# Kernel tuning notes

Measured on AMD Instinct MI355X. Metric: run time of the kernel, lower is better.

## Reference

```python
import jax, jax.numpy as jnp
import numpy as np

BN_EPS = 1e-5

def _square_distance(a, b):
    # a: (B,N,3), b: (B,M,3) -> (B,N,M) squared euclidean distance
    a2 = jnp.sum(a * a, axis=-1)[:, :, None]
    b2 = jnp.sum(b * b, axis=-1)[:, None, :]
    return a2 + b2 - 2.0 * jnp.einsum('bnd,bmd->bnm', a, b)

def _bn(x, gamma, beta, mean, var):
    # eval-mode batchnorm over channel (last) dim
    return (x - mean) * jax.lax.rsqrt(var + BN_EPS) * gamma + beta

def setup_inputs() -> dict:
    key = jax.random.key(0)
    ks = jax.random.split(key, 16)
    B, M, N, D, C = 4, 2048, 16384, 64, 64
    din, dout = C + D, 64
    return {
        'xyz_down': jax.random.normal(ks[0], (B, M, 3), jnp.float32),
        'xyz_up': jax.random.normal(ks[1], (B, N, 3), jnp.float32),
        'feat_down': jax.random.normal(ks[2], (B, M, D), jnp.float32),
        'feat_up': jax.random.normal(ks[3], (B, N, C), jnp.float32),
        'W1': jax.random.normal(ks[4], (din, din), jnp.float32) * 0.05,
        'b1': jax.random.normal(ks[5], (din,), jnp.float32) * 0.05,
        'bn1_gamma': jax.random.uniform(ks[6], (din,), jnp.float32, 0.5, 1.5),
        'bn1_beta': jax.random.normal(ks[7], (din,), jnp.float32) * 0.05,
        'bn1_mean': jax.random.normal(ks[8], (din,), jnp.float32) * 0.05,
        'bn1_var': jax.random.uniform(ks[9], (din,), jnp.float32, 0.5, 1.5),
        'W2': jax.random.normal(ks[10], (dout, din), jnp.float32) * 0.05,
        'b2': jax.random.normal(ks[11], (dout,), jnp.float32) * 0.05,
        'bn2_gamma': jax.random.uniform(ks[12], (dout,), jnp.float32, 0.5, 1.5),
        'bn2_beta': jax.random.normal(ks[13], (dout,), jnp.float32) * 0.05,
        'bn2_mean': jax.random.normal(ks[14], (dout,), jnp.float32) * 0.05,
        'bn2_var': jax.random.uniform(ks[15], (dout,), jnp.float32, 0.5, 1.5),
    }

def reference(xyz_down, xyz_up, feat_down, feat_up,
              W1, b1, bn1_gamma, bn1_beta, bn1_mean, bn1_var,
              W2, b2, bn2_gamma, bn2_beta, bn2_mean, bn2_var):
    dist = _square_distance(xyz_up, xyz_down)              # (B,N,M)
    dist_recip = 1.0 / (dist + 1e-8)
    weight = dist_recip / jnp.sum(dist_recip, axis=2, keepdims=True)
    # bmm-equivalent of the original broadcast-multiply-sum
    feat_interp = jnp.einsum('bnm,bmd->bnd', weight, feat_down)  # (B,N,D)
    x = jnp.concatenate([feat_up, feat_interp], axis=-1)   # (B,N,C+D)
    # Conv1d(k=1) == pointwise linear over channel dim
    x = jnp.einsum('bnc,oc->bno', x, W1) + b1
    x = jax.nn.relu(_bn(x, bn1_gamma, bn1_beta, bn1_mean, bn1_var))
    x = jnp.einsum('bnc,oc->bno', x, W2) + b2
    x = _bn(x, bn2_gamma, bn2_beta, bn2_mean, bn2_var)
    return x
```

## Files before the change

### kernel.cpp

```cpp
#include <hip/hip_runtime.h>

typedef unsigned short u16;
typedef unsigned int   u32;
typedef unsigned long long u64;

typedef __attribute__((ext_vector_type(8))) short bf16x8;
typedef __attribute__((ext_vector_type(4))) float f32x4;
typedef __attribute__((ext_vector_type(2))) float f32x2;

#define BB 4
#define MM 2048
#define NN 16384
#define DD 64

__device__ __forceinline__ u16 f2bf(float f) {
    union { float f; u32 u; } v; v.f = f;
    u32 r = v.u + 0x7fffu + ((v.u >> 16) & 1u);
    return (u16)(r >> 16);
}

__device__ __forceinline__ u32 pack_trunc(float hi, float lo) {
    union { float f; u32 u; } a, b; a.f = hi; b.f = lo;
    return __builtin_amdgcn_perm(a.u, b.u, 0x07060302);
}

__device__ __forceinline__ u32 pack_rne(float hi, float lo) {
    return (u32)f2bf(lo) | ((u32)f2bf(hi) << 16);
}

__device__ __forceinline__ bf16x8 pack8(float4 p, float4 q) {
    bf16x8 v;
    v[0] = (short)f2bf(p.x); v[1] = (short)f2bf(p.y);
    v[2] = (short)f2bf(p.z); v[3] = (short)f2bf(p.w);
    v[4] = (short)f2bf(q.x); v[5] = (short)f2bf(q.y);
    v[6] = (short)f2bf(q.z); v[7] = (short)f2bf(q.w);
    return v;
}

#define OFF_FDT   0ull
#define OFF_XYZP  1048576ull
#define OFF_W1S   1179648ull
#define OFF_W2S   1212416ull
#define OFF_BN    1228800ull
#define WS_NEED   1230336ull

__global__ __launch_bounds__(256)
void prep6_kernel(const float* __restrict__ xyz_down,
                  const float* __restrict__ feat_down,
                  const float* __restrict__ W1, const float* __restrict__ b1,
                  const float* __restrict__ g1, const float* __restrict__ be1,
                  const float* __restrict__ m1, const float* __restrict__ v1,
                  const float* __restrict__ W2, const float* __restrict__ b2,
                  const float* __restrict__ g2, const float* __restrict__ be2,
                  const float* __restrict__ m2, const float* __restrict__ v2,
                  u16* __restrict__ fdT, float4* __restrict__ xyzP,
                  u16* __restrict__ w1s, u16* __restrict__ w2s,
                  float* __restrict__ bnbuf)
{
    const int blk = blockIdx.x, t = threadIdx.x;
    if (blk < 256) {
        __shared__ u16 T[32 * 72];
        const int b = blk >> 6, m0 = (blk & 63) * 32;
        {
            const int row = t >> 3, seg = (t & 7) * 8;
            const float4* src = (const float4*)(feat_down + ((size_t)(b * MM + m0 + row)) * 64 + seg);
            float4 v0 = src[0], v1 = src[1];
            bf16x8 pk = pack8(v0, v1);
            *(bf16x8*)&T[row * 72 + seg] = pk;
        }
        __syncthreads();
        {
            const int d = t & 63, w = t >> 6;
            union { u16 h[8]; uint4 q; } o;
#pragma unroll
            for (int j = 0; j < 8; j++) o.h[j] = T[(w * 8 + j) * 72 + d];
            *(uint4*)&fdT[((size_t)(b * 64 + d)) * MM + m0 + w * 8] = o.q;
        }
    } else if (blk < 272) {
        int g = (blk - 256) * 256 + t;
        int b = g >> 10, p = g & 1023;
        const float* s = xyz_down + ((size_t)b * MM + 2 * p) * 3;
        float x0 = s[0], y0 = s[1], z0 = s[2];
        float x1 = s[3], y1 = s[4], z1 = s[5];
        float w0 = x0 * x0 + y0 * y0 + z0 * z0 + 1e-8f;
        float w1v = x1 * x1 + y1 * y1 + z1 * z1 + 1e-8f;
        xyzP[(size_t)g * 2 + 0] = make_float4(-2.f * x0, -2.f * x1, -2.f * y0, -2.f * y1);
        xyzP[(size_t)g * 2 + 1] = make_float4(-2.f * z0, -2.f * z1, w0, w1v);
    } else if (blk < 280) {
        int slot = (blk - 272) * 256 + t;
        int f = slot >> 6, l = slot & 63;
        int kg = f >> 3, ot = f & 7;
        int o = ot * 16 + (l & 15), c = kg * 32 + (l >> 4) * 8;
        const float4* src = (const float4*)(W1 + (size_t)o * 128 + c);
        bf16x8 v = pack8(src[0], src[1]);
        *(bf16x8*)&w1s[(size_t)slot * 8] = v;
    } else if (blk < 284) {
        int slot = (blk - 280) * 256 + t;
        int f = slot >> 6, l = slot & 63;
        int kg = f >> 2, ot = f & 3;
        int o = ot * 16 + (l & 15), c = kg * 32 + (l >> 4) * 8;
        const float4* src = (const float4*)(W2 + (size_t)o * 128 + c);
        bf16x8 v = pack8(src[0], src[1]);
        *(bf16x8*)&w2s[(size_t)slot * 8] = v;
    } else {
        if (t < 128) {
            float a = g1[t] * rsqrtf(v1[t] + 1e-5f);
            bnbuf[t] = a;
            bnbuf[128 + t] = (b1[t] - m1[t]) * a + be1[t];
        } else if (t < 192) {
            int o = t - 128;
            float a = g2[o] * rsqrtf(v2[o] + 1e-5f);
            bnbuf[256 + o] = a;
            bnbuf[320 + o] = (b2[o] - m2[o]) * a + be2[o];
        }
    }
}

__global__ __launch_bounds__(512, 4)
void fused8_kernel(const float* __restrict__ xyz_up,
                   const u16* __restrict__ fdT,
                   const float4* __restrict__ xyzP,
                   const float* __restrict__ feat_up,
                   const u16* __restrict__ w1s,
                   const u16* __restrict__ w2s,
                   const float* __restrict__ bnbuf,
                   float* __restrict__ out)
{
    __shared__ __align__(16) char smem[34816];
    __shared__ float bnl[384];
    u16*   const ftbuf = (u16*)smem;
    float* const xyzb  = (float*)(smem + 18432);
    u16*   const xh    = (u16*)smem;
    float* const of    = (float*)smem;

    const int tid  = threadIdx.x;
    const int b    = blockIdx.x >> 7;
    const int n0   = (blockIdx.x & 127) * 128;
    const int wave = tid >> 6;
    const int lane = tid & 63;
    const int q    = lane >> 4;
    const int nl   = lane & 15;
    const int rg   = wave & 3;
    const int h    = wave >> 2;

    if (tid < 384) bnl[tid] = bnbuf[tid];

    float ax[2], ay[2], az[2];
    f32x2 a22[2];
#pragma unroll
    for (int rt = 0; rt < 2; rt++) {
        const int row = n0 + rg * 32 + rt * 16 + nl;
        const float* xu = xyz_up + ((size_t)(b * NN + row)) * 3;
        ax[rt] = xu[0]; ay[rt] = xu[1]; az[rt] = xu[2];
        float a2 = ax[rt] * ax[rt] + ay[rt] * ay[rt] + az[rt] * az[rt];
        a22[rt] = (f32x2){a2, a2};
    }
    const f32x2 eps2 = (f32x2){1e-8f, 1e-8f};

    f32x4 acc[2][4];
#pragma unroll
    for (int rt = 0; rt < 2; rt++)
#pragma unroll
        for (int i = 0; i < 4; i++) acc[rt][i] = (f32x4){0.f, 0.f, 0.f, 0.f};
    f32x4 accd[2];
    accd[0] = (f32x4){0.f, 0.f, 0.f, 0.f};
    accd[1] = (f32x4){0.f, 0.f, 0.f, 0.f};

    bf16x8 ones;
#pragma unroll
    for (int i = 0; i < 8; i++) ones[i] = (short)0x3F80;

    const int sd = tid >> 3, sms = (tid & 7) * 8;
    const u16* fsrc = fdT + ((size_t)(b * 64 + sd)) * MM + sms;
    const float4* xsrc = xyzP + ((size_t)b * 1024 + (tid >> 1)) * 2 + (tid & 1);

    {
        *(uint4*)&ftbuf[sd * 72 + sms] = *(const uint4*)fsrc;
        if (tid < 64)
            *(float4*)&xyzb[(tid >> 1) * 12 + (tid & 1) * 4] = xsrc[0];
    }
    __syncthreads();

    for (int c = 0; c < 32; ++c) {
        const int cur = c & 1, nxt = cur ^ 1;
        const bool have_next = (c + 1) < 32;
        uint4 nf; float4 nx;
        if (have_next) {
            nf = *(const uint4*)(fsrc + (c + 1) * 64);
            if (tid < 64) nx = xsrc[(size_t)(c + 1) * 64];
        }

        u32 fr[2][4];
#pragma unroll
        for (int jp = 0; jp < 4; jp++) {
            const int pi = h * 16 + q * 4 + jp;
            const float* base = &xyzb[cur * 384 + pi * 12];
            float4 ld0 = *(const float4*)(base);
            float4 ld1 = *(const float4*)(base + 4);
            f32x2 px = (f32x2){ld0.x, ld0.y};
            f32x2 py = (f32x2){ld0.z, ld0.w};
            f32x2 pz = (f32x2){ld1.x, ld1.y};
            f32x2 pw = (f32x2){ld1.z, ld1.w};
#pragma unroll
            for (int rt = 0; rt < 2; rt++) {
                f32x2 d = __builtin_elementwise_fma(px, (f32x2){ax[rt], ax[rt]},
                          __builtin_elementwise_fma(py, (f32x2){ay[rt], ay[rt]},
                          __builtin_elementwise_fma(pz, (f32x2){az[rt], az[rt]},
                                                    pw + a22[rt])));
                d = __builtin_elementwise_max(d, eps2);
                float r0 = __builtin_amdgcn_rcpf(d.x);
                float r1 = __builtin_amdgcn_rcpf(d.y);
                fr[rt][jp] = pack_trunc(r1, r0);
            }
        }
        bf16x8 bb[4];
#pragma unroll
        for (int dt = 0; dt < 4; dt++)
            bb[dt] = *(bf16x8*)&ftbuf[cur * 4608 + (dt * 16 + nl) * 72 + h * 32 + q * 8];
#pragma unroll
        for (int rt = 0; rt < 2; rt++) {
            union { u32 u[4]; bf16x8 v; } af;
            af.u[0] = fr[rt][0]; af.u[1] = fr[rt][1];
            af.u[2] = fr[rt][2]; af.u[3] = fr[rt][3];
#pragma unroll
            for (int dt = 0; dt < 4; dt++)
                acc[rt][dt] = __builtin_amdgcn_mfma_f32_16x16x32_bf16(af.v, bb[dt], acc[rt][dt], 0, 0, 0);
            accd[rt] = __builtin_amdgcn_mfma_f32_16x16x32_bf16(af.v, ones, accd[rt], 0, 0, 0);
        }

        if (have_next) {
            *(uint4*)&ftbuf[nxt * 4608 + sd * 72 + sms] = nf;
            if (tid < 64)
                *(float4*)&xyzb[nxt * 384 + (tid >> 1) * 12 + (tid & 1) * 4] = nx;
        }
        __syncthreads();
    }

    const int fur = tid >> 2, fsg = (tid & 3) * 16;
    const float4* fup = (const float4*)(feat_up + ((size_t)(b * NN + n0 + fur)) * 64 + fsg);
    float4 f0 = fup[0], f1 = fup[1], f2 = fup[2], f3 = fup[3];

    if (h) {
#pragma unroll
        for (int rt = 0; rt < 2; rt++)
#pragma unroll
        for (int reg = 0; reg < 4; reg++) {
            int row = rg * 32 + rt * 16 + q * 4 + reg;
#pragma unroll
            for (int dt = 0; dt < 4; dt++)
                of[row * 68 + dt * 16 + nl] = acc[rt][dt][reg];
            if (nl == 0) of[row * 68 + 64] = accd[rt][reg];
        }
    }
    __syncthreads();
    if (!h) {
#pragma unroll
        for (int rt = 0; rt < 2; rt++)
#pragma unroll
        for (int reg = 0; reg < 4; reg++) {
            int row = rg * 32 + rt * 16 + q * 4 + reg;
#pragma unroll
            for (int dt = 0; dt < 4; dt++)
                acc[rt][dt][reg] += of[row * 68 + dt * 16 + nl];
            accd[rt][reg] += of[row * 68 + 64];
        }
    }
    __syncthreads();
    if (!h) {
#pragma unroll
        for (int rt = 0; rt < 2; rt++)
#pragma unroll
        for (int reg = 0; reg < 4; reg++) {
            float inv = 1.0f / accd[rt][reg];
            int row = rg * 32 + rt * 16 + q * 4 + reg;
#pragma unroll
            for (int dt = 0; dt < 4; dt++)
                xh[row * 136 + 64 + dt * 16 + nl] = f2bf(acc[rt][dt][reg] * inv);
        }
    }
    {
        uint4 o0, o1;
        o0.x = pack_rne(f0.y, f0.x); o0.y = pack_rne(f0.w, f0.z);
        o0.z = pack_rne(f1.y, f1.x); o0.w = pack_rne(f1.w, f1.z);
        o1.x = pack_rne(f2.y, f2.x); o1.y = pack_rne(f2.w, f2.z);
        o1.z = pack_rne(f3.y, f3.x); o1.w = pack_rne(f3.w, f3.z);
        uint4* xd = (uint4*)&xh[fur * 136 + fsg];
        xd[0] = o0; xd[1] = o1;
    }
    __syncthreads();

    f32x4 acc1[8];
#pragma unroll
    for (int i = 0; i < 8; i++) acc1[i] = (f32x4){0.f, 0.f, 0.f, 0.f};
#pragma unroll
    for (int kg = 0; kg < 4; kg++) {
        bf16x8 afr = *(bf16x8*)&xh[(wave * 16 + nl) * 136 + kg * 32 + q * 8];
#pragma unroll
        for (int ot = 0; ot < 8; ot++) {
            bf16x8 bf = *(const bf16x8*)(w1s + ((size_t)(kg * 8 + ot) * 64 + lane) * 8);
            acc1[ot] = __builtin_amdgcn_mfma_f32_16x16x32_bf16(afr, bf, acc1[ot], 0, 0, 0);
        }
    }
#pragma unroll
    for (int ot = 0; ot < 8; ot++) {
        int o = ot * 16 + nl;
        float aa = bnl[o], bc = bnl[128 + o];
#pragma unroll
        for (int reg = 0; reg < 4; reg++) {
            float v = fmaxf(fmaf(acc1[ot][reg], aa, bc), 0.f);
            xh[(wave * 16 + q * 4 + reg) * 136 + o] = f2bf(v);
        }
    }

    f32x4 acc2[4];
#pragma unroll
    for (int i = 0; i < 4; i++) acc2[i] = (f32x4){0.f, 0.f, 0.f, 0.f};
#pragma unroll
    for (int kg = 0; kg < 4; kg++) {
        bf16x8 afr = *(bf16x8*)&xh[(wave * 16 + nl) * 136 + kg * 32 + q * 8];
#pragma unroll
        for (int ot = 0; ot < 4; ot++) {
            bf16x8 bf = *(const bf16x8*)(w2s + ((size_t)(kg * 4 + ot) * 64 + lane) * 8);
            acc2[ot] = __builtin_amdgcn_mfma_f32_16x16x32_bf16(afr, bf, acc2[ot], 0, 0, 0);
        }
    }
#pragma unroll
    for (int ot = 0; ot < 4; ot++) {
        int o = ot * 16 + nl;
        float aa = bnl[256 + o], bc = bnl[320 + o];
#pragma unroll
        for (int reg = 0; reg < 4; reg++)
            of[(wave * 16 + q * 4 + reg) * 68 + o] = fmaf(acc2[ot][reg], aa, bc);
    }

    {
        const float4* sf = (const float4*)&of[fur * 68 + fsg];
        float4* dst = (float4*)(out + ((size_t)(b * NN + n0 + fur)) * 64 + fsg);
#pragma unroll
        for (int i = 0; i < 4; i++) dst[i] = sf[i];
    }
}

#define TN 128
#define BM 64
#define RS 72
#define FS 72

__global__ __launch_bounds__(256, 3)
void interp_kernel(const float* __restrict__ xyz_down,
                   const float* __restrict__ xyz_up,
                   const float* __restrict__ feat_down,
                   u16* __restrict__ interp_out)
{
    __shared__ u16   rbuf[TN * RS];
    __shared__ u16   ftbuf[DD * FS];
    __shared__ float xyzb[BM * 3];
    __shared__ float denp[TN * 2];
    __shared__ float invden[TN];

    const int tid = threadIdx.x;
    const int b  = blockIdx.x >> 7;
    const int n0 = (blockIdx.x & 127) * TN;

    const int nl_r = tid >> 1;
    const int half = tid & 1;
    const float* xu = xyz_up + (size_t)(b * NN + n0 + nl_r) * 3;
    const float ax = xu[0], ay = xu[1], az = xu[2];

    denp[tid] = 0.f;

    const int wave = tid >> 6;
    const int lane = tid & 63;
    const int q    = lane >> 4;
    const int nl   = lane & 15;

    f32x4 acc[2][4];
#pragma unroll
    for (int i = 0; i < 2; i++)
#pragma unroll
        for (int j = 0; j < 4; j++) acc[i][j] = (f32x4){0.f, 0.f, 0.f, 0.f};

    const int sm = (tid & 31) * 2;
    const int sd = (tid >> 5) * 8;

    for (int mc = 0; mc < MM; mc += BM) {
        __syncthreads();
        if (tid < 192) xyzb[tid] = xyz_down[(size_t)(b * MM + mc) * 3 + tid];
        {
            const float4* f0 = (const float4*)(feat_down + (size_t)(b * MM + mc + sm) * DD + sd);
            const float4* f1 = (const float4*)(feat_down + (size_t)(b * MM + mc + sm + 1) * DD + sd);
            float4 a0 = f0[0], a1 = f0[1];
            float4 b0 = f1[0], b1 = f1[1];
            float r0[8] = {a0.x, a0.y, a0.z, a0.w, a1.x, a1.y, a1.z, a1.w};
            float r1[8] = {b0.x, b0.y, b0.z, b0.w, b1.x, b1.y, b1.z, b1.w};
#pragma unroll
            for (int j = 0; j < 8; j++) {
                u32 pk = (u32)f2bf(r0[j]) | ((u32)f2bf(r1[j]) << 16);
                *(u32*)&ftbuf[(sd + j) * FS + sm] = pk;
            }
        }
        __syncthreads();
        {
            float dlc = 0.f;
#pragma unroll
            for (int s = 0; s < 4; s++) {
                bf16x8 v;
#pragma unroll
                for (int j = 0; j < 8; j++) {
                    int m = half * 32 + s * 8 + j;
                    float dx = ax - xyzb[3 * m + 0];
                    float dy = ay - xyzb[3 * m + 1];
                    float dz = az - xyzb[3 * m + 2];
                    float d = fmaf(dx, dx, fmaf(dy, dy, dz * dz)) + 1e-8f;
                    float r = __builtin_amdgcn_rcpf(d);
                    dlc += r;
                    v[j] = (short)f2bf(r);
                }
                *(bf16x8*)&rbuf[nl_r * RS + half * 32 + s * 8] = v;
            }
            denp[nl_r * 2 + half] += dlc;
        }
        __syncthreads();
        {
            const int rowbase = wave * 32;
#pragma unroll
            for (int k0 = 0; k0 < BM; k0 += 32) {
                bf16x8 a0 = *(bf16x8*)&rbuf[(rowbase + nl) * RS + k0 + q * 8];
                bf16x8 a1 = *(bf16x8*)&rbuf[(rowbase + 16 + nl) * RS + k0 + q * 8];
#pragma unroll
                for (int dt = 0; dt < 4; dt++) {
                    bf16x8 bb = *(bf16x8*)&ftbuf[(dt * 16 + nl) * FS + k0 + q * 8];
                    acc[0][dt] = __builtin_amdgcn_mfma_f32_16x16x32_bf16(a0, bb, acc[0][dt], 0, 0, 0);
                    acc[1][dt] = __builtin_amdgcn_mfma_f32_16x16x32_bf16(a1, bb, acc[1][dt], 0, 0, 0);
                }
            }
        }
    }

    __syncthreads();
    if (tid < TN) invden[tid] = 1.0f / (denp[tid * 2] + denp[tid * 2 + 1]);
    __syncthreads();
    {
        const int rowbase = wave * 32;
#pragma unroll
        for (int nt = 0; nt < 2; nt++) {
#pragma unroll
            for (int reg = 0; reg < 4; reg++) {
                int nloc = rowbase + nt * 16 + q * 4 + reg;
                float inv = invden[nloc];
                size_t gbase = (size_t)(b * NN + n0 + nloc) * DD;
#pragma unroll
                for (int dt = 0; dt < 4; dt++)
                    interp_out[gbase + dt * 16 + nl] = f2bf(acc[nt][dt][reg] * inv);
            }
        }
    }
}

#define T2 64

__global__ __launch_bounds__(256, 1)
void mlp_kernel(const float* __restrict__ feat_up,
                const u16*   __restrict__ interp,
                const float* __restrict__ W1, const float* __restrict__ b1,
                const float* __restrict__ g1, const float* __restrict__ be1,
                const float* __restrict__ m1, const float* __restrict__ v1,
                const float* __restrict__ W2, const float* __restrict__ b2,
                const float* __restrict__ g2, const float* __restrict__ be2,
                const float* __restrict__ m2, const float* __restrict__ v2,
                float* __restrict__ out)
{
    __shared__ u16 xb[T2 * 136];
    __shared__ u16 hb[T2 * 136];
    __shared__ u16 w1b[128 * 136];
    __shared__ u16 w2b[64 * 136];
    __shared__ float A1[128], Bc1[128], A2[64], Bc2[64];

    const int tid = threadIdx.x;
    const int b  = blockIdx.x >> 8;
    const int n0 = (blockIdx.x & 255) * T2;
    const int wave = tid >> 6;
    const int lane = tid & 63;
    const int q    = lane >> 4;
    const int nl   = lane & 15;

    if (tid < 128) {
        float a = g1[tid] * rsqrtf(v1[tid] + 1e-5f);
        A1[tid]  = a;
        Bc1[tid] = (b1[tid] - m1[tid]) * a + be1[tid];
    } else if (tid < 192) {
        int o = tid - 128;
        float a = g2[o] * rsqrtf(v2[o] + 1e-5f);
        A2[o]  = a;
        Bc2[o] = (b2[o] - m2[o]) * a + be2[o];
    }
    {
        const float4* src = (const float4*)(W1 + (size_t)(tid >> 1) * 128 + (tid & 1) * 64);
        u16* dst = &w1b[(tid >> 1) * 136 + (tid & 1) * 64];
#pragma unroll
        for (int i = 0; i < 8; i++)
            *(bf16x8*)(dst + 8 * i) = pack8(src[2 * i], src[2 * i + 1]);
    }
    {
        const float4* src = (const float4*)(W2 + (size_t)(tid >> 2) * 128 + (tid & 3) * 32);
        u16* dst = &w2b[(tid >> 2) * 136 + (tid & 3) * 32];
#pragma unroll
        for (int i = 0; i < 4; i++)
            *(bf16x8*)(dst + 8 * i) = pack8(src[2 * i], src[2 * i + 1]);
    }
    if (tid < 128) {
        int n = tid >> 1, hf = tid & 1;
        const float4* src = (const float4*)(feat_up + (size_t)(b * NN + n0 + n) * 64 + hf * 32);
        u16* dst = &xb[n * 136 + hf * 32];
#pragma unroll
        for (int i = 0; i < 4; i++)
            *(bf16x8*)(dst + 8 * i) = pack8(src[2 * i], src[2 * i + 1]);
    } else {
        int t2 = tid - 128;
        int n = t2 >> 1, hf = t2 & 1;
        const uint4* src = (const uint4*)(interp + (size_t)(b * NN + n0 + n) * 64 + hf * 32);
        u16* dst = &xb[n * 136 + 64 + hf * 32];
#pragma unroll
        for (int i = 0; i < 4; i++)
            *(uint4*)(dst + 8 * i) = src[i];
    }
    __syncthreads();

    f32x4 acc1[8];
#pragma unroll
    for (int i = 0; i < 8; i++) acc1[i] = (f32x4){0.f, 0.f, 0.f, 0.f};
#pragma unroll
    for (int k0 = 0; k0 < 128; k0 += 32) {
        bf16x8 a = *(bf16x8*)&xb[(wave * 16 + nl) * 136 + k0 + q * 8];
#pragma unroll
        for (int ot = 0; ot < 8; ot++) {
            bf16x8 bb = *(bf16x8*)&w1b[(ot * 16 + nl) * 136 + k0 + q * 8];
            acc1[ot] = __builtin_amdgcn_mfma_f32_16x16x32_bf16(a, bb, acc1[ot], 0, 0, 0);
        }
    }
#pragma unroll
    for (int ot = 0; ot < 8; ot++) {
        int o = ot * 16 + nl;
        float aa = A1[o], bc = Bc1[o];
#pragma unroll
        for (int reg = 0; reg < 4; reg++) {
            float v = fmaxf(fmaf(acc1[ot][reg], aa, bc), 0.f);
            hb[(wave * 16 + q * 4 + reg) * 136 + o] = f2bf(v);
        }
    }
    __syncthreads();

    f32x4 acc2[4];
#pragma unroll
    for (int i = 0; i < 4; i++) acc2[i] = (f32x4){0.f, 0.f, 0.f, 0.f};
#pragma unroll
    for (int k0 = 0; k0 < 128; k0 += 32) {
        bf16x8 a = *(bf16x8*)&hb[(wave * 16 + nl) * 136 + k0 + q * 8];
#pragma unroll
        for (int ot = 0; ot < 4; ot++) {
            bf16x8 bb = *(bf16x8*)&w2b[(ot * 16 + nl) * 136 + k0 + q * 8];
            acc2[ot] = __builtin_amdgcn_mfma_f32_16x16x32_bf16(a, bb, acc2[ot], 0, 0, 0);
        }
    }
#pragma unroll
    for (int ot = 0; ot < 4; ot++) {
        int o = ot * 16 + nl;
        float aa = A2[o], bc = Bc2[o];
#pragma unroll
        for (int reg = 0; reg < 4; reg++)
            out[(size_t)(b * NN + n0 + wave * 16 + q * 4 + reg) * 64 + o] =
                fmaf(acc2[ot][reg], aa, bc);
    }
}

extern "C" void kernel_launch(void* const* d_in, const int* in_sizes, int n_in,
                              void* d_out, int out_size, void* d_ws, size_t ws_size,
                              hipStream_t stream) {
    const float* xyz_down  = (const float*)d_in[0];
    const float* xyz_up    = (const float*)d_in[1];
    const float* feat_down = (const float*)d_in[2];
    const float* feat_up   = (const float*)d_in[3];
    const float* W1  = (const float*)d_in[4];
    const float* b1  = (const float*)d_in[5];
    const float* g1  = (const float*)d_in[6];
    const float* be1 = (const float*)d_in[7];
    const float* m1  = (const float*)d_in[8];
    const float* v1  = (const float*)d_in[9];
    const float* W2  = (const float*)d_in[10];
    const float* b2  = (const float*)d_in[11];
    const float* g2  = (const float*)d_in[12];
    const float* be2 = (const float*)d_in[13];
    const float* m2  = (const float*)d_in[14];
    const float* v2  = (const float*)d_in[15];
    float* out = (float*)d_out;
    char* ws = (char*)d_ws;

    if (ws_size >= WS_NEED) {
        u16*    fdT   = (u16*)(ws + OFF_FDT);
        float4* xyzP  = (float4*)(ws + OFF_XYZP);
        u16*    w1s   = (u16*)(ws + OFF_W1S);
        u16*    w2s   = (u16*)(ws + OFF_W2S);
        float*  bnbuf = (float*)(ws + OFF_BN);

        prep6_kernel<<<dim3(285), dim3(256), 0, stream>>>(
            xyz_down, feat_down, W1, b1, g1, be1, m1, v1,
            W2, b2, g2, be2, m2, v2, fdT, xyzP, w1s, w2s, bnbuf);
        fused8_kernel<<<dim3(BB * (NN / 128)), dim3(512), 0, stream>>>(
            xyz_up, fdT, xyzP, feat_up, w1s, w2s, bnbuf, out);
    } else {
        u16* interp = (u16*)d_ws;
        interp_kernel<<<dim3(BB * (NN / TN)), dim3(256), 0, stream>>>(
            xyz_down, xyz_up, feat_down, interp);
        mlp_kernel<<<dim3(BB * (NN / T2)), dim3(256), 0, stream>>>(
            feat_up, interp, W1, b1, g1, be1, m1, v1,
            W2, b2, g2, be2, m2, v2, out);
    }
}
```

Measured before the change: 145.1 us.

## Preload all xyz points to LDS and stream feature B-fragments from global

The whole batch's packed xyz_down table (2048 points, 32 KB) is loaded into shared memory once, split into two float4 arrays. The per-chunk LDS double-buffering and the per-iteration __syncthreads are removed. Feature-down MFMA B operands are now read straight from global memory into registers, with a one-chunk register prefetch. This drops the barrier per chunk and the LDS staging of features, but every wave now issues its own strided global loads (mostly L2 hits), and the larger up-front LDS fill could reduce occupancy.

```diff
diff --git a/kernel.cpp b/kernel.cpp
--- a/kernel.cpp
+++ b/kernel.cpp
@@ -117,7 +117,7 @@
 }
 
 __global__ __launch_bounds__(512, 4)
-void fused8_kernel(const float* __restrict__ xyz_up,
+void fused9_kernel(const float* __restrict__ xyz_up,
                    const u16* __restrict__ fdT,
                    const float4* __restrict__ xyzP,
                    const float* __restrict__ feat_up,
@@ -128,10 +128,10 @@
 {
     __shared__ __align__(16) char smem[34816];
     __shared__ float bnl[384];
-    u16*   const ftbuf = (u16*)smem;
-    float* const xyzb  = (float*)(smem + 18432);
-    u16*   const xh    = (u16*)smem;
-    float* const of    = (float*)smem;
+    float4* const xzA = (float4*)smem;
+    float4* const xzB = (float4*)smem + 1024;
+    u16*   const xh   = (u16*)smem;
+    float* const of   = (float*)smem;
 
     const int tid  = threadIdx.x;
     const int b    = blockIdx.x >> 7;
@@ -145,6 +145,17 @@
 
     if (tid < 384) bnl[tid] = bnbuf[tid];
 
+    {
+        const float4* src = xyzP + (size_t)b * 2048;
+#pragma unroll
+        for (int k = 0; k < 4; k++) {
+            int idx = tid + k * 512;
+            float4 v = src[idx];
+            int pair = idx >> 1;
+            if (idx & 1) xzB[pair] = v; else xzA[pair] = v;
+        }
+    }
+
     float ax[2], ay[2], az[2];
     f32x2 a22[2];
 #pragma unroll
@@ -170,33 +181,27 @@
 #pragma unroll
     for (int i = 0; i < 8; i++) ones[i] = (short)0x3F80;
 
-    const int sd = tid >> 3, sms = (tid & 7) * 8;
-    const u16* fsrc = fdT + ((size_t)(b * 64 + sd)) * MM + sms;
-    const float4* xsrc = xyzP + ((size_t)b * 1024 + (tid >> 1)) * 2 + (tid & 1);
-
-    {
-        *(uint4*)&ftbuf[sd * 72 + sms] = *(const uint4*)fsrc;
-        if (tid < 64)
-            *(float4*)&xyzb[(tid >> 1) * 12 + (tid & 1) * 4] = xsrc[0];
-    }
-    __syncthreads();
+    __syncthreads();
+
+    const u16* fdb = fdT + (size_t)b * 64 * MM + h * 32 + q * 8;
+    bf16x8 bbc[4], bbn[4];
+#pragma unroll
+    for (int dt = 0; dt < 4; dt++)
+        bbc[dt] = *(const bf16x8*)(fdb + (size_t)(dt * 16 + nl) * MM);
 
     for (int c = 0; c < 32; ++c) {
-        const int cur = c & 1, nxt = cur ^ 1;
-        const bool have_next = (c + 1) < 32;
-        uint4 nf; float4 nx;
-        if (have_next) {
-            nf = *(const uint4*)(fsrc + (c + 1) * 64);
-            if (tid < 64) nx = xsrc[(size_t)(c + 1) * 64];
+        if (c + 1 < 32) {
+#pragma unroll
+            for (int dt = 0; dt < 4; dt++)
+                bbn[dt] = *(const bf16x8*)(fdb + (size_t)(dt * 16 + nl) * MM + (c + 1) * 64);
         }
 
         u32 fr[2][4];
 #pragma unroll
         for (int jp = 0; jp < 4; jp++) {
-            const int pi = h * 16 + q * 4 + jp;
-            const float* base = &xyzb[cur * 384 + pi * 12];
-            float4 ld0 = *(const float4*)(base);
-            float4 ld1 = *(const float4*)(base + 4);
+            const int pi = c * 32 + h * 16 + q * 4 + jp;
+            float4 ld0 = xzA[pi];
+            float4 ld1 = xzB[pi];
             f32x2 px = (f32x2){ld0.x, ld0.y};
             f32x2 py = (f32x2){ld0.z, ld0.w};
             f32x2 pz = (f32x2){ld1.x, ld1.y};
@@ -213,10 +218,6 @@
                 fr[rt][jp] = pack_trunc(r1, r0);
             }
         }
-        bf16x8 bb[4];
-#pragma unroll
-        for (int dt = 0; dt < 4; dt++)
-            bb[dt] = *(bf16x8*)&ftbuf[cur * 4608 + (dt * 16 + nl) * 72 + h * 32 + q * 8];
 #pragma unroll
         for (int rt = 0; rt < 2; rt++) {
             union { u32 u[4]; bf16x8 v; } af;
@@ -224,21 +225,18 @@
             af.u[2] = fr[rt][2]; af.u[3] = fr[rt][3];
 #pragma unroll
             for (int dt = 0; dt < 4; dt++)
-                acc[rt][dt] = __builtin_amdgcn_mfma_f32_16x16x32_bf16(af.v, bb[dt], acc[rt][dt], 0, 0, 0);
+                acc[rt][dt] = __builtin_amdgcn_mfma_f32_16x16x32_bf16(af.v, bbc[dt], acc[rt][dt], 0, 0, 0);
             accd[rt] = __builtin_amdgcn_mfma_f32_16x16x32_bf16(af.v, ones, accd[rt], 0, 0, 0);
         }
-
-        if (have_next) {
-            *(uint4*)&ftbuf[nxt * 4608 + sd * 72 + sms] = nf;
-            if (tid < 64)
-                *(float4*)&xyzb[nxt * 384 + (tid >> 1) * 12 + (tid & 1) * 4] = nx;
-        }
-        __syncthreads();
+#pragma unroll
+        for (int dt = 0; dt < 4; dt++) bbc[dt] = bbn[dt];
     }
 
     const int fur = tid >> 2, fsg = (tid & 3) * 16;
     const float4* fup = (const float4*)(feat_up + ((size_t)(b * NN + n0 + fur)) * 64 + fsg);
     float4 f0 = fup[0], f1 = fup[1], f2 = fup[2], f3 = fup[3];
+
+    __syncthreads();
 
     if (h) {
 #pragma unroll
@@ -605,7 +603,7 @@
         prep6_kernel<<<dim3(285), dim3(256), 0, stream>>>(
             xyz_down, feat_down, W1, b1, g1, be1, m1, v1,
             W2, b2, g2, be2, m2, v2, fdT, xyzP, w1s, w2s, bnbuf);
-        fused8_kernel<<<dim3(BB * (NN / 128)), dim3(512), 0, stream>>>(
+        fused9_kernel<<<dim3(BB * (NN / 128)), dim3(512), 0, stream>>>(
             xyz_up, fdT, xyzP, feat_up, w1s, w2s, bnbuf, out);
     } else {
         u16* interp = (u16*)d_ws;
```

Result: slower. 168.2 us (+15.9%).

## Prefetch two chunks ahead and replace syncthreads with lgkmcnt-only barrier

Applied to the files above, without the earlier changes.

The interpolation loop now keeps the next chunk in registers and issues global loads two iterations ahead, writing the register-held chunk into the spare LDS buffer at the start of each iteration. The per-iteration __syncthreads is replaced by an LDS-only wait (s_waitcnt lgkmcnt(0)) plus s_barrier, wrapped in sched_barrier. Global loads no longer have to complete before the barrier, so memory latency can overlap the distance and MFMA work of the current chunk. The trade-off is extra live registers for the prefetched data and hand-written synchronisation that relies on the LDS write and read ordering being correct.

```diff
diff --git a/kernel.cpp b/kernel.cpp
--- a/kernel.cpp
+++ b/kernel.cpp
@@ -117,14 +117,14 @@
 }
 
 __global__ __launch_bounds__(512, 4)
-void fused8_kernel(const float* __restrict__ xyz_up,
-                   const u16* __restrict__ fdT,
-                   const float4* __restrict__ xyzP,
-                   const float* __restrict__ feat_up,
-                   const u16* __restrict__ w1s,
-                   const u16* __restrict__ w2s,
-                   const float* __restrict__ bnbuf,
-                   float* __restrict__ out)
+void fused10_kernel(const float* __restrict__ xyz_up,
+                    const u16* __restrict__ fdT,
+                    const float4* __restrict__ xyzP,
+                    const float* __restrict__ feat_up,
+                    const u16* __restrict__ w1s,
+                    const u16* __restrict__ w2s,
+                    const float* __restrict__ bnbuf,
+                    float* __restrict__ out)
 {
     __shared__ __align__(16) char smem[34816];
     __shared__ float bnl[384];
@@ -173,21 +173,37 @@
     const int sd = tid >> 3, sms = (tid & 7) * 8;
     const u16* fsrc = fdT + ((size_t)(b * 64 + sd)) * MM + sms;
     const float4* xsrc = xyzP + ((size_t)b * 1024 + (tid >> 1)) * 2 + (tid & 1);
+    const int xoff = (tid >> 1) * 12 + (tid & 1) * 4;
+
+    uint4  rf;
+    float4 rx;
 
     {
-        *(uint4*)&ftbuf[sd * 72 + sms] = *(const uint4*)fsrc;
-        if (tid < 64)
-            *(float4*)&xyzb[(tid >> 1) * 12 + (tid & 1) * 4] = xsrc[0];
-    }
-    __syncthreads();
-
+        uint4 f0v = *(const uint4*)(fsrc);
+        *(uint4*)&ftbuf[sd * 72 + sms] = f0v;
+        if (tid < 64) {
+            float4 x0 = xsrc[0];
+            *(float4*)&xyzb[xoff] = x0;
+        }
+        rf = *(const uint4*)(fsrc + 64);
+        if (tid < 64) rx = xsrc[64];
+        __builtin_amdgcn_sched_barrier(0);
+        asm volatile("s_waitcnt lgkmcnt(0)" ::: "memory");
+        __builtin_amdgcn_s_barrier();
+        __builtin_amdgcn_sched_barrier(0);
+    }
+
+    int cur = 0;
     for (int c = 0; c < 32; ++c) {
-        const int cur = c & 1, nxt = cur ^ 1;
-        const bool have_next = (c + 1) < 32;
-        uint4 nf; float4 nx;
-        if (have_next) {
-            nf = *(const uint4*)(fsrc + (c + 1) * 64);
-            if (tid < 64) nx = xsrc[(size_t)(c + 1) * 64];
+        const int nxt = cur ^ 1;
+
+        if (c + 1 < 32) {
+            *(uint4*)&ftbuf[nxt * 4608 + sd * 72 + sms] = rf;
+            if (tid < 64) *(float4*)&xyzb[nxt * 384 + xoff] = rx;
+        }
+        if (c + 2 < 32) {
+            rf = *(const uint4*)(fsrc + (size_t)(c + 2) * 64);
+            if (tid < 64) rx = xsrc[(size_t)(c + 2) * 64];
         }
 
         u32 fr[2][4];
@@ -228,12 +244,11 @@
             accd[rt] = __builtin_amdgcn_mfma_f32_16x16x32_bf16(af.v, ones, accd[rt], 0, 0, 0);
         }
 
-        if (have_next) {
-            *(uint4*)&ftbuf[nxt * 4608 + sd * 72 + sms] = nf;
-            if (tid < 64)
-                *(float4*)&xyzb[nxt * 384 + (tid >> 1) * 12 + (tid & 1) * 4] = nx;
-        }
-        __syncthreads();
+        __builtin_amdgcn_sched_barrier(0);
+        asm volatile("s_waitcnt lgkmcnt(0)" ::: "memory");
+        __builtin_amdgcn_s_barrier();
+        __builtin_amdgcn_sched_barrier(0);
+        cur = nxt;
     }
 
     const int fur = tid >> 2, fsg = (tid & 3) * 16;
@@ -605,7 +620,7 @@
         prep6_kernel<<<dim3(285), dim3(256), 0, stream>>>(
             xyz_down, feat_down, W1, b1, g1, be1, m1, v1,
             W2, b2, g2, be2, m2, v2, fdT, xyzP, w1s, w2s, bnbuf);
-        fused8_kernel<<<dim3(BB * (NN / 128)), dim3(512), 0, stream>>>(
+        fused10_kernel<<<dim3(BB * (NN / 128)), dim3(512), 0, stream>>>(
             xyz_up, fdT, xyzP, feat_up, w1s, w2s, bnbuf, out);
     } else {
         u16* interp = (u16*)d_ws;
```

Measured after the change: 146.3 us. Within noise of the previous version (+0.8%).
